# Kernel optimization log

Hardware: AMD Instinct MI355X
Metric: run time of the kernel (lower is better)

## Reference

```python
import jax, jax.numpy as jnp
import numpy as np

DIM = 1024
H = 16
HD = DIM // H


def setup_inputs() -> dict:
    key = jax.random.key(0)
    ks = jax.random.split(key, 14)
    B, L1, L2 = 8, 512, 512
    s = 0.02
    return {
        "seq1": jax.random.normal(ks[0], (B, L1, DIM), jnp.float32),
        "seq2": jax.random.normal(ks[1], (B, L2, DIM), jnp.float32),
        "atc1": jax.random.normal(ks[2], (B, L1, 5), jnp.float32),
        "atc2": jax.random.normal(ks[3], (B, L2, 5), jnp.float32),
        "Wq": jax.random.normal(ks[4], (DIM, DIM), jnp.float32) * s,
        "bq": jnp.zeros((DIM,), jnp.float32),
        "Wk": jax.random.normal(ks[5], (DIM, DIM), jnp.float32) * s,
        "bk": jnp.zeros((DIM,), jnp.float32),
        "Wv": jax.random.normal(ks[6], (DIM, DIM), jnp.float32) * s,
        "bv": jnp.zeros((DIM,), jnp.float32),
        "Wo": jax.random.normal(ks[7], (DIM, DIM), jnp.float32) * s,
        "bo": jnp.zeros((DIM,), jnp.float32),
        "U": jax.random.normal(ks[8], (H, 5, 5), jnp.float32) * 0.02,
        "mix_param": jnp.float32(0.0),
    }


def reference(seq1, seq2, atc1, atc2, Wq, bq, Wk, bk, Wv, bv, Wo, bo, U, mix_param):
    B, L1, _ = seq1.shape
    L2 = seq2.shape[1]
    # projections; weights stored (out,in) like nn.Linear -> x @ W.T + b
    q = (seq1 @ Wq.T + bq).reshape(B, L1, H, HD).transpose(0, 2, 1, 3)  # b h l1 d
    k = (seq2 @ Wk.T + bk).reshape(B, L2, H, HD).transpose(0, 2, 1, 3)
    v = (seq2 @ Wv.T + bv).reshape(B, L2, H, HD).transpose(0, 2, 1, 3)
    std_scores = jnp.einsum('bhid,bhjd->bhij', q, k) / jnp.sqrt(jnp.float32(HD))
    # per-head Atchley bias: bip, hpq, bjq -> bhij (vectorized over heads)
    bio_scores = jnp.einsum('bip,hpq,bjq->bhij', atc1, U, atc2)
    mix = jnp.tanh(mix_param)
    mix_ratio = (mix + 1.0) / 2.0
    attn = (1.0 - mix_ratio) * jax.nn.softmax(std_scores, axis=-1) \
         + mix_ratio * jax.nn.softmax(bio_scores, axis=-1)
    out = jnp.einsum('bhij,bhjd->bhid', attn, v)  # b h l1 d
    out = out.transpose(0, 2, 1, 3).reshape(B, L1, DIM)
    return out @ Wo.T + bo
```

## Files before the change

kernel.cpp:

```cpp
#include <hip/hip_runtime.h>

typedef __attribute__((ext_vector_type(8))) short short8;
typedef __attribute__((ext_vector_type(8))) unsigned short ushort8;
typedef __attribute__((ext_vector_type(4))) float f32x4;
typedef unsigned short u16;

#define DIM 1024
#define NH 16
#define HD 64
#define NB 8
#define L 512
#define ML (NB * L)

__device__ __forceinline__ u16 f2bf(float f) {
  union { float f; unsigned int u; } x; x.f = f;
  unsigned int r = x.u + 0x7FFFu + ((x.u >> 16) & 1u);
  return (u16)(r >> 16);
}

__device__ __forceinline__ void gld16(u16* lds, const u16* g) {
  __builtin_amdgcn_global_load_lds(
      (__attribute__((address_space(1))) void*)g,
      (__attribute__((address_space(3))) void*)lds, 16, 0, 0);
}

__global__ __launch_bounds__(256) void cvt_all(
    const float* __restrict__ s1, const float* __restrict__ s2,
    const float* __restrict__ wq, const float* __restrict__ wk,
    const float* __restrict__ wv, const float* __restrict__ wo,
    u16* __restrict__ o1, u16* __restrict__ o2, u16* __restrict__ oq,
    u16* __restrict__ ok, u16* __restrict__ ov, u16* __restrict__ oo) {
  const int blk = blockIdx.x;
  const float* src; u16* dst; int rel;
  if (blk < 2048)       { src = s1; dst = o1; rel = blk; }
  else if (blk < 4096)  { src = s2; dst = o2; rel = blk - 2048; }
  else if (blk < 4608)  { src = wq; dst = oq; rel = blk - 4096; }
  else if (blk < 5120)  { src = wk; dst = ok; rel = blk - 4608; }
  else if (blk < 5632)  { src = wv; dst = ov; rel = blk - 5120; }
  else                  { src = wo; dst = oo; rel = blk - 5632; }
  const int i = rel * 256 + threadIdx.x;
  const float4 v0 = reinterpret_cast<const float4*>(src)[2 * i];
  const float4 v1 = reinterpret_cast<const float4*>(src)[2 * i + 1];
  ushort8 o;
  o[0] = f2bf(v0.x); o[1] = f2bf(v0.y); o[2] = f2bf(v0.z); o[3] = f2bf(v0.w);
  o[4] = f2bf(v1.x); o[5] = f2bf(v1.y); o[6] = f2bf(v1.z); o[7] = f2bf(v1.w);
  reinterpret_cast<ushort8*>(dst)[i] = o;
}

template <int BN, bool OUT_F32, bool KV>
__global__ __launch_bounds__(256) void gemm_lds(
    const u16* __restrict__ A, const u16* __restrict__ Bw,
    const float* __restrict__ b0, const float* __restrict__ b1,
    void* __restrict__ Cp, int M, int N, int K) {
  __shared__ __align__(16) u16 As[128 * 32];
  __shared__ __align__(16) u16 Bs[BN * 32];
  const int tid = threadIdx.x;
  const int lane = tid & 63;
  const int w = tid >> 6;
  const int ll = lane & 15, lg = lane >> 4;
  const int wm = (w >> 1) * 64;
  const int wn = (w & 1) * (BN / 2);
  constexpr int NF = BN / 32;
  const int bm = blockIdx.y * 128;
  const int bn = blockIdx.x * BN;

  f32x4 acc[4][NF];
#pragma unroll
  for (int m = 0; m < 4; ++m)
#pragma unroll
    for (int n = 0; n < NF; ++n) acc[m][n] = (f32x4){0.f, 0.f, 0.f, 0.f};

  for (int kt = 0; kt < K; kt += 32) {
#pragma unroll
    for (int it = 0; it < 2; ++it) {
      const int slot = it * 256 + tid;
      gld16(As + (it * 256 + w * 64) * 8,
            A + (size_t)(bm + (slot >> 2)) * K + kt + (slot & 3) * 8);
    }
#pragma unroll
    for (int it = 0; it < BN / 64; ++it) {
      const int slot = it * 256 + tid;
      gld16(Bs + (it * 256 + w * 64) * 8,
            Bw + (size_t)(bn + (slot >> 2)) * K + kt + (slot & 3) * 8);
    }
    __syncthreads();
    short8 af[4], bf[NF];
#pragma unroll
    for (int m = 0; m < 4; ++m)
      af[m] = *reinterpret_cast<const short8*>(&As[(wm + m * 16 + ll) * 32 + lg * 8]);
#pragma unroll
    for (int n = 0; n < NF; ++n)
      bf[n] = *reinterpret_cast<const short8*>(&Bs[(wn + n * 16 + ll) * 32 + lg * 8]);
#pragma unroll
    for (int m = 0; m < 4; ++m)
#pragma unroll
      for (int n = 0; n < NF; ++n)
        acc[m][n] = __builtin_amdgcn_mfma_f32_16x16x32_bf16(af[m], bf[n], acc[m][n], 0, 0, 0);
    __syncthreads();
  }

#pragma unroll
  for (int m = 0; m < 4; ++m) {
#pragma unroll
    for (int n = 0; n < NF; ++n) {
#pragma unroll
      for (int r = 0; r < 4; ++r) {
        const int row = bm + wm + m * 16 + lg * 4 + r;
        const int col = bn + wn + n * 16 + ll;
        float bb;
        if constexpr (KV) bb = (col < DIM) ? b0[col] : b1[col - DIM];
        else bb = b0[col];
        const float v = acc[m][n][r] + bb;
        if constexpr (OUT_F32)
          reinterpret_cast<float*>(Cp)[(size_t)row * N + col] = v;
        else
          reinterpret_cast<u16*>(Cp)[(size_t)row * N + col] = f2bf(v);
      }
    }
  }
}

__global__ __launch_bounds__(256) void transpose_v(const u16* __restrict__ kvb,
                                                   u16* __restrict__ vt) {
  __shared__ u16 T[64][65];
  const int jt = blockIdx.x, h = blockIdx.y, bb = blockIdx.z;
  const int tid = threadIdx.x;
#pragma unroll
  for (int rep = 0; rep < 16; ++rep) {
    const int idx = rep * 256 + tid;
    const int jr = idx >> 6, d = idx & 63;
    T[jr][d] = kvb[(size_t)(bb * L + jt * 64 + jr) * 2048 + DIM + h * HD + d];
  }
  __syncthreads();
#pragma unroll
  for (int rep = 0; rep < 16; ++rep) {
    const int idx = rep * 256 + tid;
    const int dr = idx >> 6, j = idx & 63;
    vt[(size_t)((bb * NH + h) * HD + dr) * L + jt * 64 + j] = T[j][dr];
  }
}

__global__ __launch_bounds__(256) void a1u_kernel(const float* __restrict__ atc1,
                                                  const float* __restrict__ U,
                                                  float* __restrict__ a1u) {
  const int idx = blockIdx.x * 256 + threadIdx.x;
  if (idx >= NB * NH * L * 5) return;
  const int q = idx % 5;
  const int i = (idx / 5) & (L - 1);
  const int h = (idx / (5 * L)) & (NH - 1);
  const int b = idx / (5 * L * NH);
  float s = 0.f;
#pragma unroll
  for (int p = 0; p < 5; ++p)
    s += atc1[(size_t)(b * L + i) * 5 + p] * U[(h * 5 + p) * 5 + q];
  a1u[idx] = s;
}

__global__ __launch_bounds__(256, 4) void attn2(
    const u16* __restrict__ qb, const u16* __restrict__ kvb,
    const u16* __restrict__ vt, const float* __restrict__ a1u,
    const float* __restrict__ atc2, const float* __restrict__ mixp,
    u16* __restrict__ attb) {
  __shared__ __align__(16) float S[16][516];
  const int tid = threadIdx.x;
  const int wv = tid >> 6;
  const int lane = tid & 63;
  const int ll = lane & 15, lg = lane >> 4;
  const int bid = blockIdx.x;
  const int slot = bid >> 3;
  const int bh = (bid & 7) * 16 + (slot >> 5);
  const int it = slot & 31;
  const int b = bh >> 4, h = bh & 15;
  const int i0 = it * 16;

  const float ratio = (tanhf(mixp[0]) + 1.0f) * 0.5f;

  const u16* qp = qb + (size_t)(b * L + i0 + ll) * DIM + h * HD + lg * 8;
  const short8 aq0 = *reinterpret_cast<const short8*>(qp);
  const short8 aq1 = *reinterpret_cast<const short8*>(qp + 32);

  float au[4][5];
#pragma unroll
  for (int ri = 0; ri < 4; ++ri) {
    const float* ap = a1u + (size_t)((b * NH + h) * L + i0 + wv * 4 + ri) * 5;
#pragma unroll
    for (int p = 0; p < 5; ++p) au[ri][p] = ap[p];
  }
  float bs[4][8];
#pragma unroll
  for (int t = 0; t < 8; ++t) {
    const int j = lane + 64 * t;
    const float* c2 = atc2 + (size_t)(b * L + j) * 5;
    const float c0 = c2[0], c1 = c2[1], cc2 = c2[2], c3 = c2[3], c4 = c2[4];
#pragma unroll
    for (int ri = 0; ri < 4; ++ri)
      bs[ri][t] = au[ri][0] * c0 + au[ri][1] * c1 + au[ri][2] * cc2 +
                  au[ri][3] * c3 + au[ri][4] * c4;
  }

#pragma unroll 2
  for (int jt = 0; jt < 8; ++jt) {
    const int jj = wv * 8 + jt;
    const u16* kp = kvb + (size_t)(b * L + jj * 16 + ll) * 2048 + h * HD + lg * 8;
    const short8 k0 = *reinterpret_cast<const short8*>(kp);
    const short8 k1 = *reinterpret_cast<const short8*>(kp + 32);
    f32x4 s = (f32x4){0.f, 0.f, 0.f, 0.f};
    s = __builtin_amdgcn_mfma_f32_16x16x32_bf16(aq0, k0, s, 0, 0, 0);
    s = __builtin_amdgcn_mfma_f32_16x16x32_bf16(aq1, k1, s, 0, 0, 0);
#pragma unroll
    for (int r = 0; r < 4; ++r) S[lg * 4 + r][jj * 16 + ll] = s[r] * 0.125f;
  }
  __syncthreads();

#pragma unroll
  for (int ri = 0; ri < 4; ++ri) {
    const int i = wv * 4 + ri;
    float v1[8];
    float m1 = -1e30f;
#pragma unroll
    for (int t = 0; t < 8; ++t) { v1[t] = S[i][lane + 64 * t]; m1 = fmaxf(m1, v1[t]); }
#pragma unroll
    for (int off = 32; off > 0; off >>= 1) m1 = fmaxf(m1, __shfl_xor(m1, off));
    float e1[8];
    float l1 = 0.f;
#pragma unroll
    for (int t = 0; t < 8; ++t) { e1[t] = __expf(v1[t] - m1); l1 += e1[t]; }
#pragma unroll
    for (int off = 32; off > 0; off >>= 1) l1 += __shfl_xor(l1, off);
    float m2 = -1e30f;
#pragma unroll
    for (int t = 0; t < 8; ++t) m2 = fmaxf(m2, bs[ri][t]);
#pragma unroll
    for (int off = 32; off > 0; off >>= 1) m2 = fmaxf(m2, __shfl_xor(m2, off));
    float e2[8];
    float l2 = 0.f;
#pragma unroll
    for (int t = 0; t < 8; ++t) { e2[t] = __expf(bs[ri][t] - m2); l2 += e2[t]; }
#pragma unroll
    for (int off = 32; off > 0; off >>= 1) l2 += __shfl_xor(l2, off);
    const float sc1 = (1.f - ratio) / l1, sc2 = ratio / l2;
#pragma unroll
    for (int t = 0; t < 8; ++t) S[i][lane + 64 * t] = sc1 * e1[t] + sc2 * e2[t];
  }
  __syncthreads();

  f32x4 O = (f32x4){0.f, 0.f, 0.f, 0.f};
  const u16* vbase = vt + ((size_t)(b * NH + h) * HD + wv * 16 + ll) * L;
#pragma unroll 4
  for (int kk = 0; kk < 16; ++kk) {
    const float* pr = &S[ll][kk * 32 + lg * 8];
    const float4 p0 = *reinterpret_cast<const float4*>(pr);
    const float4 p1 = *reinterpret_cast<const float4*>(pr + 4);
    short8 pa;
    pa[0] = (short)f2bf(p0.x); pa[1] = (short)f2bf(p0.y);
    pa[2] = (short)f2bf(p0.z); pa[3] = (short)f2bf(p0.w);
    pa[4] = (short)f2bf(p1.x); pa[5] = (short)f2bf(p1.y);
    pa[6] = (short)f2bf(p1.z); pa[7] = (short)f2bf(p1.w);
    const short8 bv = *reinterpret_cast<const short8*>(vbase + kk * 32 + lg * 8);
    O = __builtin_amdgcn_mfma_f32_16x16x32_bf16(pa, bv, O, 0, 0, 0);
  }
#pragma unroll
  for (int r = 0; r < 4; ++r)
    attb[(size_t)(b * L + i0 + lg * 4 + r) * DIM + h * HD + wv * 16 + ll] = f2bf(O[r]);
}

extern "C" void kernel_launch(void* const* d_in, const int* in_sizes, int n_in,
                              void* d_out, int out_size, void* d_ws, size_t ws_size,
                              hipStream_t stream) {
  (void)in_sizes; (void)n_in; (void)out_size; (void)ws_size;
  const float* seq1 = (const float*)d_in[0];
  const float* seq2 = (const float*)d_in[1];
  const float* atc1 = (const float*)d_in[2];
  const float* atc2 = (const float*)d_in[3];
  const float* Wq = (const float*)d_in[4];
  const float* bq = (const float*)d_in[5];
  const float* Wk = (const float*)d_in[6];
  const float* bk = (const float*)d_in[7];
  const float* Wv = (const float*)d_in[8];
  const float* bv = (const float*)d_in[9];
  const float* Wo = (const float*)d_in[10];
  const float* bo = (const float*)d_in[11];
  const float* U = (const float*)d_in[12];
  const float* mixp = (const float*)d_in[13];

  char* ws = (char*)d_ws;
  const size_t SEQB = (size_t)ML * DIM * sizeof(u16);
  const size_t WB = (size_t)DIM * DIM * sizeof(u16);
  size_t o = 0;
  u16* s1b = (u16*)(ws + o); o += SEQB;
  u16* s2b = (u16*)(ws + o); o += SEQB;
  u16* wqb = (u16*)(ws + o); o += WB;
  u16* wkvb = (u16*)(ws + o); o += 2 * WB;
  u16* wob = (u16*)(ws + o); o += WB;
  u16* qb = (u16*)(ws + o); o += SEQB;
  u16* kvb = (u16*)(ws + o); o += 2 * SEQB;
  u16* vtb = (u16*)(ws + o); o += SEQB;
  u16* attb = (u16*)(ws + o); o += SEQB;
  float* a1u = (float*)(ws + o); o += (size_t)NB * NH * L * 5 * sizeof(float);

  cvt_all<<<6144, 256, 0, stream>>>(seq1, seq2, Wq, Wk, Wv, Wo, s1b, s2b, wqb,
                                    wkvb, wkvb + (size_t)DIM * DIM, wob);

  gemm_lds<64, false, false><<<dim3(16, 32), 256, 0, stream>>>(
      s1b, wqb, bq, bq, qb, ML, DIM, DIM);
  gemm_lds<128, false, true><<<dim3(16, 32), 256, 0, stream>>>(
      s2b, wkvb, bk, bv, kvb, ML, 2048, DIM);

  transpose_v<<<dim3(L / 64, NH, NB), 256, 0, stream>>>(kvb, vtb);
  a1u_kernel<<<(NB * NH * L * 5 + 255) / 256, 256, 0, stream>>>(atc1, U, a1u);

  attn2<<<4096, 256, 0, stream>>>(qb, kvb, vtb, a1u, atc2, mixp, attb);

  gemm_lds<64, true, false><<<dim3(16, 32), 256, 0, stream>>>(
      attb, wob, bo, bo, (float*)d_out, ML, DIM, DIM);
}
```

Baseline: 265.5 us.

## Double-buffer GEMM tiles and streamline attention softmax with bf16 LDS probabilities

Result: faster. 259.0 us (-2.4%).

```diff
diff --git a/kernel.cpp b/kernel.cpp
--- a/kernel.cpp
+++ b/kernel.cpp
@@ -1,4 +1,5 @@
 #include <hip/hip_runtime.h>
+#include <hip/hip_bf16.h>
 
 typedef __attribute__((ext_vector_type(8))) short short8;
 typedef __attribute__((ext_vector_type(8))) unsigned short ushort8;
@@ -16,6 +17,12 @@
   union { float f; unsigned int u; } x; x.f = f;
   unsigned int r = x.u + 0x7FFFu + ((x.u >> 16) & 1u);
   return (u16)(r >> 16);
+}
+
+__device__ __forceinline__ unsigned int pkbf(float a, float b) {
+  union { __hip_bfloat162 h; unsigned int u; } r;
+  r.h = __float22bfloat162_rn(float2{a, b});
+  return r.u;
 }
 
 __device__ __forceinline__ void gld16(u16* lds, const u16* g) {
@@ -47,13 +54,13 @@
   reinterpret_cast<ushort8*>(dst)[i] = o;
 }
 
-template <int BN, bool OUT_F32, bool KV>
-__global__ __launch_bounds__(256) void gemm_lds(
+template <int BN, bool OUT_F32, bool KV, int NT>
+__global__ __launch_bounds__(256) void gemm_db(
     const u16* __restrict__ A, const u16* __restrict__ Bw,
     const float* __restrict__ b0, const float* __restrict__ b1,
-    void* __restrict__ Cp, int M, int N, int K) {
-  __shared__ __align__(16) u16 As[128 * 32];
-  __shared__ __align__(16) u16 Bs[BN * 32];
+    void* __restrict__ Cp, int N, int K) {
+  __shared__ __align__(16) u16 As[2][128 * 32];
+  __shared__ __align__(16) u16 Bs[2][BN * 32];
   const int tid = threadIdx.x;
   const int lane = tid & 63;
   const int w = tid >> 6;
@@ -61,8 +68,10 @@
   const int wm = (w >> 1) * 64;
   const int wn = (w & 1) * (BN / 2);
   constexpr int NF = BN / 32;
-  const int bm = blockIdx.y * 128;
-  const int bn = blockIdx.x * BN;
+  const int bid = blockIdx.x;
+  const int tile = (bid & 7) * (gridDim.x >> 3) + (bid >> 3);
+  const int bm = (tile / NT) * 128;
+  const int bn = (tile % NT) * BN;
 
   f32x4 acc[4][NF];
 #pragma unroll
@@ -70,33 +79,40 @@
 #pragma unroll
     for (int n = 0; n < NF; ++n) acc[m][n] = (f32x4){0.f, 0.f, 0.f, 0.f};
 
-  for (int kt = 0; kt < K; kt += 32) {
+  auto stage = [&](int bi, int kt) {
 #pragma unroll
     for (int it = 0; it < 2; ++it) {
       const int slot = it * 256 + tid;
-      gld16(As + (it * 256 + w * 64) * 8,
+      gld16(&As[bi][(it * 256 + w * 64) * 8],
             A + (size_t)(bm + (slot >> 2)) * K + kt + (slot & 3) * 8);
     }
 #pragma unroll
     for (int it = 0; it < BN / 64; ++it) {
       const int slot = it * 256 + tid;
-      gld16(Bs + (it * 256 + w * 64) * 8,
+      gld16(&Bs[bi][(it * 256 + w * 64) * 8],
             Bw + (size_t)(bn + (slot >> 2)) * K + kt + (slot & 3) * 8);
     }
-    __syncthreads();
+  };
+
+  stage(0, 0);
+  __syncthreads();
+  int cur = 0;
+  for (int kt = 0; kt < K; kt += 32) {
+    if (kt + 32 < K) stage(cur ^ 1, kt + 32);
     short8 af[4], bf[NF];
 #pragma unroll
     for (int m = 0; m < 4; ++m)
-      af[m] = *reinterpret_cast<const short8*>(&As[(wm + m * 16 + ll) * 32 + lg * 8]);
+      af[m] = *reinterpret_cast<const short8*>(&As[cur][(wm + m * 16 + ll) * 32 + lg * 8]);
 #pragma unroll
     for (int n = 0; n < NF; ++n)
-      bf[n] = *reinterpret_cast<const short8*>(&Bs[(wn + n * 16 + ll) * 32 + lg * 8]);
+      bf[n] = *reinterpret_cast<const short8*>(&Bs[cur][(wn + n * 16 + ll) * 32 + lg * 8]);
 #pragma unroll
     for (int m = 0; m < 4; ++m)
 #pragma unroll
       for (int n = 0; n < NF; ++n)
         acc[m][n] = __builtin_amdgcn_mfma_f32_16x16x32_bf16(af[m], bf[n], acc[m][n], 0, 0, 0);
     __syncthreads();
+    cur ^= 1;
   }
 
 #pragma unroll
@@ -156,12 +172,12 @@
   a1u[idx] = s;
 }
 
-__global__ __launch_bounds__(256, 4) void attn2(
+__global__ __launch_bounds__(256, 4) void attn3(
     const u16* __restrict__ qb, const u16* __restrict__ kvb,
     const u16* __restrict__ vt, const float* __restrict__ a1u,
     const float* __restrict__ atc2, const float* __restrict__ mixp,
     u16* __restrict__ attb) {
-  __shared__ __align__(16) float S[16][516];
+  __shared__ __align__(16) float Sf[16 * 512];
   const int tid = threadIdx.x;
   const int wv = tid >> 6;
   const int lane = tid & 63;
@@ -179,83 +195,93 @@
   const short8 aq0 = *reinterpret_cast<const short8*>(qp);
   const short8 aq1 = *reinterpret_cast<const short8*>(qp + 32);
 
-  float au[4][5];
-#pragma unroll
-  for (int ri = 0; ri < 4; ++ri) {
-    const float* ap = a1u + (size_t)((b * NH + h) * L + i0 + wv * 4 + ri) * 5;
-#pragma unroll
-    for (int p = 0; p < 5; ++p) au[ri][p] = ap[p];
-  }
   float bs[4][8];
-#pragma unroll
-  for (int t = 0; t < 8; ++t) {
-    const int j = lane + 64 * t;
-    const float* c2 = atc2 + (size_t)(b * L + j) * 5;
-    const float c0 = c2[0], c1 = c2[1], cc2 = c2[2], c3 = c2[3], c4 = c2[4];
-#pragma unroll
-    for (int ri = 0; ri < 4; ++ri)
-      bs[ri][t] = au[ri][0] * c0 + au[ri][1] * c1 + au[ri][2] * cc2 +
-                  au[ri][3] * c3 + au[ri][4] * c4;
-  }
-
-#pragma unroll 2
-  for (int jt = 0; jt < 8; ++jt) {
-    const int jj = wv * 8 + jt;
+  {
+    float r2a[20], r2b[20];
+    {
+      const float4* pa = reinterpret_cast<const float4*>(atc2 + ((size_t)b * L + 4 * lane) * 5);
+      const float4* pb = reinterpret_cast<const float4*>(atc2 + ((size_t)b * L + 256 + 4 * lane) * 5);
+#pragma unroll
+      for (int u = 0; u < 5; ++u) {
+        const float4 ta = pa[u], tb = pb[u];
+        r2a[4 * u] = ta.x; r2a[4 * u + 1] = ta.y; r2a[4 * u + 2] = ta.z; r2a[4 * u + 3] = ta.w;
+        r2b[4 * u] = tb.x; r2b[4 * u + 1] = tb.y; r2b[4 * u + 2] = tb.z; r2b[4 * u + 3] = tb.w;
+      }
+    }
+    const float* a1p = a1u + ((size_t)(b * NH + h) * L + i0 + wv * 4) * 5;
+    float a1v[20];
+#pragma unroll
+    for (int p = 0; p < 20; ++p) a1v[p] = a1p[p];
+#pragma unroll
+    for (int ri = 0; ri < 4; ++ri) {
+#pragma unroll
+      for (int j = 0; j < 4; ++j) {
+        float sa = 0.f, sb = 0.f;
+#pragma unroll
+        for (int p = 0; p < 5; ++p) {
+          sa += a1v[ri * 5 + p] * r2a[j * 5 + p];
+          sb += a1v[ri * 5 + p] * r2b[j * 5 + p];
+        }
+        bs[ri][j] = sa; bs[ri][j + 4] = sb;
+      }
+    }
+  }
+
+#pragma unroll
+  for (int jt8 = 0; jt8 < 8; ++jt8) {
+    const int jj = wv * 8 + jt8;
     const u16* kp = kvb + (size_t)(b * L + jj * 16 + ll) * 2048 + h * HD + lg * 8;
     const short8 k0 = *reinterpret_cast<const short8*>(kp);
     const short8 k1 = *reinterpret_cast<const short8*>(kp + 32);
     f32x4 s = (f32x4){0.f, 0.f, 0.f, 0.f};
     s = __builtin_amdgcn_mfma_f32_16x16x32_bf16(aq0, k0, s, 0, 0, 0);
     s = __builtin_amdgcn_mfma_f32_16x16x32_bf16(aq1, k1, s, 0, 0, 0);
-#pragma unroll
-    for (int r = 0; r < 4; ++r) S[lg * 4 + r][jj * 16 + ll] = s[r] * 0.125f;
+    const int cfb = jj * 4 + (ll >> 2);
+#pragma unroll
+    for (int r = 0; r < 4; ++r) {
+      const int row = lg * 4 + r;
+      Sf[row * 512 + (((cfb ^ (row & 7)) << 2) | (ll & 3))] = s[r] * 0.125f;
+    }
   }
   __syncthreads();
 
 #pragma unroll
   for (int ri = 0; ri < 4; ++ri) {
     const int i = wv * 4 + ri;
-    float v1[8];
-    float m1 = -1e30f;
-#pragma unroll
-    for (int t = 0; t < 8; ++t) { v1[t] = S[i][lane + 64 * t]; m1 = fmaxf(m1, v1[t]); }
-#pragma unroll
-    for (int off = 32; off > 0; off >>= 1) m1 = fmaxf(m1, __shfl_xor(m1, off));
-    float e1[8];
-    float l1 = 0.f;
-#pragma unroll
-    for (int t = 0; t < 8; ++t) { e1[t] = __expf(v1[t] - m1); l1 += e1[t]; }
-#pragma unroll
-    for (int off = 32; off > 0; off >>= 1) l1 += __shfl_xor(l1, off);
-    float m2 = -1e30f;
-#pragma unroll
-    for (int t = 0; t < 8; ++t) m2 = fmaxf(m2, bs[ri][t]);
-#pragma unroll
-    for (int off = 32; off > 0; off >>= 1) m2 = fmaxf(m2, __shfl_xor(m2, off));
-    float e2[8];
-    float l2 = 0.f;
-#pragma unroll
-    for (int t = 0; t < 8; ++t) { e2[t] = __expf(bs[ri][t] - m2); l2 += e2[t]; }
-#pragma unroll
-    for (int off = 32; off > 0; off >>= 1) l2 += __shfl_xor(l2, off);
+    const int p1 = lane ^ (i & 7);
+    const float4 x1 = *reinterpret_cast<const float4*>(&Sf[i * 512 + (p1 << 2)]);
+    const float4 x2 = *reinterpret_cast<const float4*>(&Sf[i * 512 + ((64 + p1) << 2)]);
+    float e1[8], e2[8];
+    e1[0] = __expf(x1.x); e1[1] = __expf(x1.y); e1[2] = __expf(x1.z); e1[3] = __expf(x1.w);
+    e1[4] = __expf(x2.x); e1[5] = __expf(x2.y); e1[6] = __expf(x2.z); e1[7] = __expf(x2.w);
+#pragma unroll
+    for (int j = 0; j < 8; ++j) e2[j] = __expf(bs[ri][j]);
+    float l1 = 0.f, l2 = 0.f;
+#pragma unroll
+    for (int j = 0; j < 8; ++j) { l1 += e1[j]; l2 += e2[j]; }
+#pragma unroll
+    for (int off = 32; off > 0; off >>= 1) {
+      l1 += __shfl_xor(l1, off);
+      l2 += __shfl_xor(l2, off);
+    }
     const float sc1 = (1.f - ratio) / l1, sc2 = ratio / l2;
-#pragma unroll
-    for (int t = 0; t < 8; ++t) S[i][lane + 64 * t] = sc1 * e1[t] + sc2 * e2[t];
+    float p[8];
+#pragma unroll
+    for (int j = 0; j < 8; ++j) p[j] = sc1 * e1[j] + sc2 * e2[j];
+    char* rowb = reinterpret_cast<char*>(Sf) + i * 2048;
+    uint2 w0; w0.x = pkbf(p[0], p[1]); w0.y = pkbf(p[2], p[3]);
+    uint2 w1; w1.x = pkbf(p[4], p[5]); w1.y = pkbf(p[6], p[7]);
+    *reinterpret_cast<uint2*>(rowb + 8 * lane) = w0;
+    *reinterpret_cast<uint2*>(rowb + 512 + 8 * lane) = w1;
   }
   __syncthreads();
 
   f32x4 O = (f32x4){0.f, 0.f, 0.f, 0.f};
   const u16* vbase = vt + ((size_t)(b * NH + h) * HD + wv * 16 + ll) * L;
-#pragma unroll 4
+  const char* Pb = reinterpret_cast<const char*>(Sf) + ll * 2048;
+#pragma unroll
   for (int kk = 0; kk < 16; ++kk) {
-    const float* pr = &S[ll][kk * 32 + lg * 8];
-    const float4 p0 = *reinterpret_cast<const float4*>(pr);
-    const float4 p1 = *reinterpret_cast<const float4*>(pr + 4);
-    short8 pa;
-    pa[0] = (short)f2bf(p0.x); pa[1] = (short)f2bf(p0.y);
-    pa[2] = (short)f2bf(p0.z); pa[3] = (short)f2bf(p0.w);
-    pa[4] = (short)f2bf(p1.x); pa[5] = (short)f2bf(p1.y);
-    pa[6] = (short)f2bf(p1.z); pa[7] = (short)f2bf(p1.w);
+    const short8 pa = *reinterpret_cast<const short8*>(Pb + kk * 64 + lg * 16);
     const short8 bv = *reinterpret_cast<const short8*>(vbase + kk * 32 + lg * 8);
     O = __builtin_amdgcn_mfma_f32_16x16x32_bf16(pa, bv, O, 0, 0, 0);
   }
@@ -301,16 +327,13 @@
   cvt_all<<<6144, 256, 0, stream>>>(seq1, seq2, Wq, Wk, Wv, Wo, s1b, s2b, wqb,
                                     wkvb, wkvb + (size_t)DIM * DIM, wob);
 
-  gemm_lds<64, false, false><<<dim3(16, 32), 256, 0, stream>>>(
-      s1b, wqb, bq, bq, qb, ML, DIM, DIM);
-  gemm_lds<128, false, true><<<dim3(16, 32), 256, 0, stream>>>(
-      s2b, wkvb, bk, bv, kvb, ML, 2048, DIM);
+  gemm_db<64, false, false, 16><<<512, 256, 0, stream>>>(s1b, wqb, bq, bq, qb, DIM, DIM);
+  gemm_db<128, false, true, 16><<<512, 256, 0, stream>>>(s2b, wkvb, bk, bv, kvb, 2048, DIM);
 
   transpose_v<<<dim3(L / 64, NH, NB), 256, 0, stream>>>(kvb, vtb);
   a1u_kernel<<<(NB * NH * L * 5 + 255) / 256, 256, 0, stream>>>(atc1, U, a1u);
 
-  attn2<<<4096, 256, 0, stream>>>(qb, kvb, vtb, a1u, atc2, mixp, attb);
-
-  gemm_lds<64, true, false><<<dim3(16, 32), 256, 0, stream>>>(
-      attb, wob, bo, bo, (float*)d_out, ML, DIM, DIM);
-}
+  attn3<<<4096, 256, 0, stream>>>(qb, kvb, vtb, a1u, atc2, mixp, attb);
+
+  gemm_db<64, true, false, 16><<<512, 256, 0, stream>>>(attb, wob, bo, bo, (float*)d_out, DIM, DIM);
+}
```
